# Kernel tuning notes

Hardware: AMD Instinct MI355X
Metric: run time of the kernel (lower is better)

Reference implementation:

```python
import jax, jax.numpy as jnp
import numpy as np
from jax import lax

R = 2  # upscale factor


def setup_inputs() -> dict:
    key = jax.random.key(0)
    k1, k2, k3 = jax.random.split(key, 3)
    x = jax.random.normal(k1, (16, 192, 192, 64), dtype=jnp.float32)
    # Conv2D kernel: HWIO, filters = r*r*64 = 256
    W = jax.random.normal(k2, (3, 3, 64, 256), dtype=jnp.float32) * 0.05
    b = jax.random.normal(k3, (256,), dtype=jnp.float32) * 0.05
    return {"x": x, "W": W, "b": b}


def reference(x, W, b):
    # Conv2D, stride 1, 'same' padding, NHWC/HWIO
    y = lax.conv_general_dilated(
        x, W, window_strides=(1, 1), padding="SAME",
        dimension_numbers=("NHWC", "HWIO", "NHWC")) + b
    # phase_shift: O[B, i*r+q, j*r+p, k] = y[B, i, j, k*r*r + p*r + q]
    B, a, bdim, c = y.shape
    cp = c // (R * R)
    y = y.reshape(B, a, bdim, cp, R, R)          # [B,a,b,k,p,q]
    y = jnp.transpose(y, (0, 1, 5, 2, 4, 3))     # [B,a,q,b,p,k]
    return y.reshape(B, a * R, bdim * R, cp)
```

## Files before the change

kernel.cpp:

```cpp
#include <hip/hip_runtime.h>
#include <stdint.h>

typedef short bf16x8 __attribute__((ext_vector_type(8)));
typedef float f32x4  __attribute__((ext_vector_type(4)));

#define GLOAD_LDS16(gp, lp) \
    __builtin_amdgcn_global_load_lds((const __attribute__((address_space(1))) void*)(gp), \
                                     (__attribute__((address_space(3))) void*)(lp), 16, 0, 0)

__device__ __forceinline__ uint32_t bfbits(float f) {
    uint32_t u = __builtin_bit_cast(uint32_t, f);
    u += 0x7FFFu + ((u >> 16) & 1u);
    return u >> 16;
}
__device__ __forceinline__ uint32_t pk2(float a, float b) {
    return bfbits(a) | (bfbits(b) << 16);
}

__global__ void prep_kernel(const float* __restrict__ x, short* __restrict__ xb,
                            const float* __restrict__ W, short* __restrict__ Wt) {
    const int b = blockIdx.x;
    if (b < 2048) {
        const int total = 16 * 194 * 194 * 8;
        for (int i = b * 256 + threadIdx.x; i < total; i += 2048 * 256) {
            int g  = i & 7;
            int t  = i >> 3;
            int wp = t % 194; t /= 194;
            int hp = t % 194;
            int nn = t / 194;
            uint4 r = {0u, 0u, 0u, 0u};
            if (hp >= 1 && hp <= 192 && wp >= 1 && wp <= 192) {
                const float* s = x + (((size_t)nn * 192 + (hp - 1)) * 192 + (wp - 1)) * 64 + g * 8;
                f32x4 a = __builtin_nontemporal_load((const f32x4*)s);
                f32x4 bb = __builtin_nontemporal_load((const f32x4*)(s + 4));
                r.x = pk2(a[0], a[1]); r.y = pk2(a[2], a[3]);
                r.z = pk2(bb[0], bb[1]); r.w = pk2(bb[2], bb[3]);
            }
            *(uint4*)(xb + (size_t)i * 8) = r;
        }
    } else {
        int idx = (b - 2048) * 256 + threadIdx.x;
        if (idx < 147456) {
            int t  = idx >> 14;
            int r  = idx & 16383;
            int c  = r >> 12;
            int j  = (r >> 6) & 63;
            int ic = r & 63;
            Wt[idx] = (short)bfbits(W[(t * 64 + ic) * 256 + j * 4 + c]);
        }
    }
}

#define NRING 7
#define ASLOT_B 8448
#define B_OFF   (NRING * ASLOT_B)
#define SMEM_SHORTS ((B_OFF + 2 * 8192) / 2)

__global__ __launch_bounds__(256, 2) void conv_ps_kernel(
    const short* __restrict__ xb, const short* __restrict__ Wt,
    const float* __restrict__ bias, float* __restrict__ out)
{
    __shared__ short smem[SMEM_SHORTS];

    const int tid   = threadIdx.x;
    const int lane  = tid & 63;
    const int wv    = tid >> 6;
    const int row_l = lane & 15;
    const int grp   = lane >> 4;
    const int b7    = row_l & 7;

    const int raw = blockIdx.x;
    const int lb  = (raw & 7) * 192 + (raw >> 3);
    const int c    = lb & 3;
    const int wt   = (lb >> 2) % 3;
    const int hseg = (lb / 12) % 8;
    const int n    = lb / 96;
    const int w0   = wt * 64;
    const int hbase = hseg * 24;
    const int q = c & 1, p = (c >> 1) & 1;

    const short* wsrc = Wt + c * 4096;

    auto issueB = [&](int tap, int buf) {
        #pragma unroll
        for (int r = 0; r < 2; ++r) {
            int cch = tid + r * 256;
            int j = cch >> 3, s = cch & 7, ss = s ^ (j & 7);
            GLOAD_LDS16(wsrc + tap * 16384 + j * 64 + ss * 8,
                        (char*)smem + B_OFF + buf * 8192 + (wv * 64 + r * 256) * 16);
        }
    };
    auto issueA = [&](int row) {
        int rowc = row > 192 ? 192 : row;
        int slot = (row + 1) % NRING;
        size_t rbase = ((size_t)n * 194 + (rowc + 1)) * 194;
        #pragma unroll
        for (int r = 0; r < 2; ++r) {
            int cch = wv * 132 + r * 64 + lane;
            int wpos = cch >> 3, g = cch & 7, gs = g ^ (wpos & 7);
            GLOAD_LDS16(xb + (rbase + (w0 + wpos)) * 64 + gs * 8,
                        (char*)smem + slot * ASLOT_B + (wv * 132 + r * 64) * 16);
        }
        if (lane < 4) {
            int cch = wv * 132 + 128 + lane;
            int wpos = cch >> 3, g = cch & 7, gs = g ^ (wpos & 7);
            GLOAD_LDS16(xb + (rbase + (w0 + wpos)) * 64 + gs * 8,
                        (char*)smem + slot * ASLOT_B + (wv * 132 + 128) * 16);
        }
    };

    issueB(0, 0);
    #pragma unroll
    for (int r = 0; r < 5; ++r) issueA(hbase - 1 + r);
    asm volatile("s_waitcnt vmcnt(0)" ::: "memory");
    __builtin_amdgcn_sched_barrier(0);
    __syncthreads();

    f32x4 bv4[4];
    #pragma unroll
    for (int nt = 0; nt < 4; ++nt) {
        const int j0 = nt * 16 + grp * 4;
        #pragma unroll
        for (int jv = 0; jv < 4; ++jv)
            bv4[nt][jv] = bias[(j0 + jv) * 4 + c];
    }

#define TAP_HDR() \
    __builtin_amdgcn_s_barrier(); \
    __builtin_amdgcn_sched_barrier(0);
#define TAP_SYNC(VMN) \
    __builtin_amdgcn_sched_barrier(0); \
    asm volatile("s_waitcnt vmcnt(" #VMN ")" ::: "memory"); \
    __builtin_amdgcn_sched_barrier(0); \
    __builtin_amdgcn_s_barrier(); \
    __builtin_amdgcn_sched_barrier(0);

#define COMPUTE_TAP(DY, DX, BUF) { \
    const int rd = row_l + (DX); \
    const int a7 = rd & 7; \
    const int aB = sl[DY] * 4224 + rd * 64; \
    const short* bbase = smem + B_OFF / 2 + (BUF) * 4096 + row_l * 64; \
    _Pragma("unroll") for (int ks = 0; ks < 2; ++ks) { \
        const int kg = ks * 4 + grp; \
        const short* ap = &smem[aB + ((kg ^ a7) << 3)]; \
        const short* bp = bbase + ((kg ^ b7) << 3); \
        bf16x8 af[4], bfr[4]; \
        _Pragma("unroll") for (int mt = 0; mt < 4; ++mt) af[mt]  = *(const bf16x8*)(ap + mt * 1024); \
        _Pragma("unroll") for (int nt = 0; nt < 4; ++nt) bfr[nt] = *(const bf16x8*)(bp + nt * 1024); \
        _Pragma("unroll") for (int mt = 0; mt < 4; ++mt) \
            _Pragma("unroll") for (int nt = 0; nt < 4; ++nt) \
                acc[mt][nt] = __builtin_amdgcn_mfma_f32_16x16x32_bf16( \
                    bfr[nt], af[mt], acc[mt][nt], 0, 0, 0); \
    } }

    int pb = 0;
    #pragma unroll 1
    for (int it = 0; it < 6; ++it) {
        const int h0 = hbase + it * 4;

        int sl[3];
        #pragma unroll
        for (int dy = 0; dy < 3; ++dy) sl[dy] = (h0 + wv + dy) % NRING;

        f32x4 acc[4][4];
        #pragma unroll
        for (int i = 0; i < 4; ++i)
            #pragma unroll
            for (int j = 0; j < 4; ++j)
                acc[i][j] = bv4[j];

        const int pA = pb, pBb = pb ^ 1;

        TAP_HDR();
        issueB(1, pBb); issueA(h0 + 4); issueA(h0 + 5);
        TAP_SYNC(24);
        COMPUTE_TAP(0, 0, pA);
        TAP_HDR();
        issueB(2, pA);
        TAP_SYNC(8);
        COMPUTE_TAP(0, 1, pBb);
        TAP_HDR();
        issueB(3, pBb);
        TAP_SYNC(2);
        COMPUTE_TAP(0, 2, pA);
        TAP_HDR();
        issueB(4, pA); issueA(h0 + 6);
        TAP_SYNC(5);
        COMPUTE_TAP(1, 0, pBb);
        TAP_HDR();
        issueB(5, pBb);
        TAP_SYNC(5);
        COMPUTE_TAP(1, 1, pA);
        TAP_HDR();
        issueB(6, pA);
        TAP_SYNC(2);
        COMPUTE_TAP(1, 2, pBb);
        TAP_HDR();
        issueB(7, pBb); issueA(h0 + 7);
        TAP_SYNC(5);
        COMPUTE_TAP(2, 0, pA);
        TAP_HDR();
        issueB(8, pA);
        TAP_SYNC(5);
        COMPUTE_TAP(2, 1, pBb);
        TAP_HDR();
        issueB(0, pBb);
        TAP_SYNC(2);
        COMPUTE_TAP(2, 2, pA);

        {
            const int h = h0 + wv;
            const long rowb = ((long)(n * 384 + 2 * h + q)) * 384;
            #pragma unroll
            for (int mt = 0; mt < 4; ++mt) {
                float* po = out + ((rowb + 2 * (w0 + mt * 16 + row_l) + p) * 64 + grp * 4);
                #pragma unroll
                for (int nt = 0; nt < 4; ++nt)
                    __builtin_nontemporal_store(acc[mt][nt], (f32x4*)(po + nt * 16));
            }
        }

        pb ^= 1;
    }
#undef COMPUTE_TAP
#undef TAP_HDR
#undef TAP_SYNC
}

extern "C" void kernel_launch(void* const* d_in, const int* in_sizes, int n_in,
                              void* d_out, int out_size, void* d_ws, size_t ws_size,
                              hipStream_t stream) {
    const float* x = (const float*)d_in[0];
    const float* W = (const float*)d_in[1];
    const float* b = (const float*)d_in[2];
    float* out = (float*)d_out;

    const size_t xb_bytes = (size_t)16 * 194 * 194 * 64 * 2;
    short* xbuf = (short*)d_ws;
    short* Wt   = (short*)((char*)d_ws + xb_bytes);

    hipLaunchKernelGGL(prep_kernel, dim3(2624), dim3(256), 0, stream, x, xbuf, W, Wt);
    hipLaunchKernelGGL(conv_ps_kernel, dim3(1536), dim3(256), 0, stream, xbuf, Wt, b, out);
}
```

Baseline: 236.6 us.

## Double-buffer accumulators to overlap previous tile's output stores with next tile's taps

```diff
diff --git a/kernel.cpp b/kernel.cpp
--- a/kernel.cpp
+++ b/kernel.cpp
@@ -125,17 +125,11 @@
             bv4[nt][jv] = bias[(j0 + jv) * 4 + c];
     }
 
-#define TAP_HDR() \
-    __builtin_amdgcn_s_barrier(); \
-    __builtin_amdgcn_sched_barrier(0);
-#define TAP_SYNC(VMN) \
-    __builtin_amdgcn_sched_barrier(0); \
-    asm volatile("s_waitcnt vmcnt(" #VMN ")" ::: "memory"); \
-    __builtin_amdgcn_sched_barrier(0); \
-    __builtin_amdgcn_s_barrier(); \
-    __builtin_amdgcn_sched_barrier(0);
-
-#define COMPUTE_TAP(DY, DX, BUF) { \
+    f32x4 accA[4][4], accB[4][4];
+
+#define SCHB __builtin_amdgcn_sched_barrier(0)
+
+#define COMPUTE_TAP(ACC, DY, DX, BUF) { \
     const int rd = row_l + (DX); \
     const int a7 = rd & 7; \
     const int aB = sl[DY] * 4224 + rd * 64; \
@@ -149,82 +143,80 @@
         _Pragma("unroll") for (int nt = 0; nt < 4; ++nt) bfr[nt] = *(const bf16x8*)(bp + nt * 1024); \
         _Pragma("unroll") for (int mt = 0; mt < 4; ++mt) \
             _Pragma("unroll") for (int nt = 0; nt < 4; ++nt) \
-                acc[mt][nt] = __builtin_amdgcn_mfma_f32_16x16x32_bf16( \
-                    bfr[nt], af[mt], acc[mt][nt], 0, 0, 0); \
+                ACC[mt][nt] = __builtin_amdgcn_mfma_f32_16x16x32_bf16( \
+                    bfr[nt], af[mt], ACC[mt][nt], 0, 0, 0); \
     } }
 
-    int pb = 0;
+#define ST2(ACCO, S) { \
+    const int mt_ = (S) >> 1, n0_ = ((S) & 1) * 2; \
+    float* po_ = out + ((rowb_o + 2 * (w0 + mt_ * 16 + row_l) + p) * 64 + grp * 4); \
+    __builtin_nontemporal_store(ACCO[mt_][n0_],     (f32x4*)(po_ + n0_ * 16)); \
+    __builtin_nontemporal_store(ACCO[mt_][n0_ + 1], (f32x4*)(po_ + (n0_ + 1) * 16)); }
+
+#define TAPX(ACC, K, DY, DX, PAR, VM, EXTRA, STS) \
+    __builtin_amdgcn_s_barrier(); SCHB; \
+    issueB(((K) + 1) % 9, ((PAR) + (K) + 1) & 1); \
+    EXTRA; SCHB; \
+    STS; SCHB; \
+    asm volatile("s_waitcnt vmcnt(" #VM ")" ::: "memory"); SCHB; \
+    __builtin_amdgcn_s_barrier(); SCHB; \
+    COMPUTE_TAP(ACC, DY, DX, ((PAR) + (K)) & 1)
+
+#define TILE_HEAD(ACC, ITV) \
+    const int h0 = hbase + (ITV) * 4; \
+    int sl[3]; \
+    _Pragma("unroll") for (int dy = 0; dy < 3; ++dy) sl[dy] = (h0 + wv + dy) % NRING; \
+    _Pragma("unroll") for (int i = 0; i < 4; ++i) \
+        _Pragma("unroll") for (int j = 0; j < 4; ++j) ACC[i][j] = bv4[j];
+
+#define STEADY_TILE(ACC, ACCO, ITV, PAR) { \
+    TILE_HEAD(ACC, ITV); \
+    const long rowb_o = ((long)(n * 384 + 2 * (h0 - 4 + wv) + q)) * 384; \
+    TAPX(ACC, 0, 0, 0, PAR, 10, { issueA(h0 + 4); issueA(h0 + 5); }, ST2(ACCO, 0)); \
+    TAPX(ACC, 1, 0, 1, PAR, 12, {}, ST2(ACCO, 1)); \
+    TAPX(ACC, 2, 0, 2, PAR,  6, {}, ST2(ACCO, 2)); \
+    TAPX(ACC, 3, 1, 0, PAR,  9, { issueA(h0 + 6); }, ST2(ACCO, 3)); \
+    TAPX(ACC, 4, 1, 1, PAR,  9, {}, ST2(ACCO, 4)); \
+    TAPX(ACC, 5, 1, 2, PAR,  6, {}, ST2(ACCO, 5)); \
+    TAPX(ACC, 6, 2, 0, PAR,  9, { issueA(h0 + 7); }, ST2(ACCO, 6)); \
+    TAPX(ACC, 7, 2, 1, PAR,  9, {}, ST2(ACCO, 7)); \
+    TAPX(ACC, 8, 2, 2, PAR,  4, {}, {}); }
+
+    {
+        TILE_HEAD(accA, 0);
+        TAPX(accA, 0, 0, 0, 0, 8, { issueA(h0 + 4); issueA(h0 + 5); }, {});
+        TAPX(accA, 1, 0, 1, 0, 8, {}, {});
+        TAPX(accA, 2, 0, 2, 0, 2, {}, {});
+        TAPX(accA, 3, 1, 0, 0, 5, { issueA(h0 + 6); }, {});
+        TAPX(accA, 4, 1, 1, 0, 5, {}, {});
+        TAPX(accA, 5, 1, 2, 0, 2, {}, {});
+        TAPX(accA, 6, 2, 0, 0, 5, { issueA(h0 + 7); }, {});
+        TAPX(accA, 7, 2, 1, 0, 5, {}, {});
+        TAPX(accA, 8, 2, 2, 0, 2, {}, {});
+    }
     #pragma unroll 1
-    for (int it = 0; it < 6; ++it) {
-        const int h0 = hbase + it * 4;
-
-        int sl[3];
-        #pragma unroll
-        for (int dy = 0; dy < 3; ++dy) sl[dy] = (h0 + wv + dy) % NRING;
-
-        f32x4 acc[4][4];
-        #pragma unroll
-        for (int i = 0; i < 4; ++i)
+    for (int it2 = 1; it2 < 5; it2 += 2) {
+        STEADY_TILE(accB, accA, it2, 1);
+        STEADY_TILE(accA, accB, it2 + 1, 0);
+    }
+    STEADY_TILE(accB, accA, 5, 1);
+    {
+        const int h = hbase + 20 + wv;
+        const long rowb = ((long)(n * 384 + 2 * h + q)) * 384;
+        #pragma unroll
+        for (int mt = 0; mt < 4; ++mt) {
+            float* po = out + ((rowb + 2 * (w0 + mt * 16 + row_l) + p) * 64 + grp * 4);
             #pragma unroll
-            for (int j = 0; j < 4; ++j)
-                acc[i][j] = bv4[j];
-
-        const int pA = pb, pBb = pb ^ 1;
-
-        TAP_HDR();
-        issueB(1, pBb); issueA(h0 + 4); issueA(h0 + 5);
-        TAP_SYNC(24);
-        COMPUTE_TAP(0, 0, pA);
-        TAP_HDR();
-        issueB(2, pA);
-        TAP_SYNC(8);
-        COMPUTE_TAP(0, 1, pBb);
-        TAP_HDR();
-        issueB(3, pBb);
-        TAP_SYNC(2);
-        COMPUTE_TAP(0, 2, pA);
-        TAP_HDR();
-        issueB(4, pA); issueA(h0 + 6);
-        TAP_SYNC(5);
-        COMPUTE_TAP(1, 0, pBb);
-        TAP_HDR();
-        issueB(5, pBb);
-        TAP_SYNC(5);
-        COMPUTE_TAP(1, 1, pA);
-        TAP_HDR();
-        issueB(6, pA);
-        TAP_SYNC(2);
-        COMPUTE_TAP(1, 2, pBb);
-        TAP_HDR();
-        issueB(7, pBb); issueA(h0 + 7);
-        TAP_SYNC(5);
-        COMPUTE_TAP(2, 0, pA);
-        TAP_HDR();
-        issueB(8, pA);
-        TAP_SYNC(5);
-        COMPUTE_TAP(2, 1, pBb);
-        TAP_HDR();
-        issueB(0, pBb);
-        TAP_SYNC(2);
-        COMPUTE_TAP(2, 2, pA);
-
-        {
-            const int h = h0 + wv;
-            const long rowb = ((long)(n * 384 + 2 * h + q)) * 384;
-            #pragma unroll
-            for (int mt = 0; mt < 4; ++mt) {
-                float* po = out + ((rowb + 2 * (w0 + mt * 16 + row_l) + p) * 64 + grp * 4);
-                #pragma unroll
-                for (int nt = 0; nt < 4; ++nt)
-                    __builtin_nontemporal_store(acc[mt][nt], (f32x4*)(po + nt * 16));
-            }
-        }
-
-        pb ^= 1;
-    }
+            for (int nt = 0; nt < 4; ++nt)
+                __builtin_nontemporal_store(accB[mt][nt], (f32x4*)(po + nt * 16));
+        }
+    }
+#undef STEADY_TILE
+#undef TILE_HEAD
+#undef TAPX
+#undef ST2
 #undef COMPUTE_TAP
-#undef TAP_HDR
-#undef TAP_SYNC
+#undef SCHB
 }
 
 extern "C" void kernel_launch(void* const* d_in, const int* in_sizes, int n_in,
```

Result: faster. 223.4 us (-5.6%).
